# Kernel tuning notes

Measured on AMD Instinct MI355X. Metric: run time of the kernel, lower is better.

The kernel has to match this reference:

```python
import jax, jax.numpy as jnp
import numpy as np
import math

B, C, H, T, S = 2, 1024, 16, 2048, 2048
DH = C // H  # 64


def setup_inputs() -> dict:
    key = jax.random.key(0)
    ks = jax.random.split(key, 10)
    target = jax.random.normal(ks[0], (B, C, T), dtype=jnp.float32)
    source = jax.random.normal(ks[1], (B, C, S), dtype=jnp.float32)
    target_mask = (jax.random.uniform(ks[2], (B, 1, T)) < 0.9).astype(jnp.float32)
    source_mask = (jax.random.uniform(ks[3], (B, 1, S)) < 0.9).astype(jnp.float32)
    scale = 1.0 / math.sqrt(C)
    Wq = jax.random.normal(ks[4], (C, C), dtype=jnp.float32) * scale
    bq = jnp.zeros((C,), dtype=jnp.float32)
    Wk = jax.random.normal(ks[5], (C, C), dtype=jnp.float32) * scale
    bk = jnp.zeros((C,), dtype=jnp.float32)
    Wv = jax.random.normal(ks[6], (C, C), dtype=jnp.float32) * scale
    bv = jnp.zeros((C,), dtype=jnp.float32)
    return {"target": target, "source": source, "target_mask": target_mask,
            "source_mask": source_mask, "Wq": Wq, "bq": bq, "Wk": Wk, "bk": bk,
            "Wv": Wv, "bv": bv}


def _proj(W, b, x):
    # 1x1 Conv1d == pointwise channel mixing: [B,C,L] -> [B,C,L]
    return jnp.einsum('oc,bcl->bol', W, x) + b[None, :, None]


def reference(target, source, target_mask, source_mask, Wq, bq, Wk, bk, Wv, bv):
    q = _proj(Wq, bq, target).reshape(B, H, DH, T)
    k = _proj(Wk, bk, source).reshape(B, H, DH, S)
    v = _proj(Wv, bv, source).reshape(B, H, DH, S)
    # dot: [B,H,T,S], scaled by sqrt(d_head) (key.size(2) in torch)
    dot = jnp.einsum('bhdt,bhds->bhts', q, k) / math.sqrt(DH)
    # available mask [B,1,T,S], broadcast over heads
    avail = jnp.einsum('bjt,bjs->bjts', target_mask, source_mask)
    dot = avail * dot - (1.0 - avail) * 1.0e6
    # NOTE: original torch code overwrites the masked amap with a plain
    # softmax of the (masked) dot; we reproduce that exactly.
    amap = jax.nn.softmax(dot, axis=-1)
    out = jnp.einsum('bhts,bhds->bhdt', amap, v)  # [B,H,DH,T]
    return out.reshape(B, C, T)
```

## Files before the change

### kernel.cpp

```cpp
#include <hip/hip_runtime.h>

#define BB 2
#define CC 1024
#define HH 16
#define TT 2048
#define SS 2048
#define LL 2048
#define C2MASK 1442695.0f
#define NT_TILES (SS / 64)

typedef unsigned short u16;
typedef unsigned int u32;
typedef __attribute__((ext_vector_type(8))) short short8;
typedef __attribute__((ext_vector_type(4))) float f32x4;
typedef __attribute__((ext_vector_type(4))) unsigned short us4;
typedef __attribute__((ext_vector_type(2))) unsigned int u32x2;
typedef __attribute__((ext_vector_type(4))) unsigned int u32x4;

__device__ __forceinline__ u16 f2bf(float f) {
    union { float f; unsigned int i; } x; x.f = f;
    unsigned int r = x.i + 0x7FFFu + ((x.i >> 16) & 1u);
    return (u16)(r >> 16);
}
__device__ __forceinline__ float exp2_hw(float x) {
    float r;
    asm("v_exp_f32 %0, %1" : "=v"(r) : "v"(x));
    return r;
}
__device__ __forceinline__ float max3f(float a, float b, float c) {
    float r;
    asm("v_max3_f32 %0, %1, %2, %3" : "=v"(r) : "v"(a), "v"(b), "v"(c));
    return r;
}
__device__ __forceinline__ u32 cvtpk_bf16(float lo, float hi) {
    u32 r;
    asm("v_cvt_pk_bf16_f32 %0, %1, %2" : "=v"(r) : "v"(lo), "v"(hi));
    return r;
}
__device__ __forceinline__ void gload_lds16(const u16* g, u16* l) {
    __builtin_amdgcn_global_load_lds(
        (const __attribute__((address_space(1))) unsigned int*)g,
        (__attribute__((address_space(3))) unsigned int*)l, 16, 0, 0);
}

__global__ __launch_bounds__(256) void prep(
    const float* __restrict__ target, const float* __restrict__ source,
    const float* __restrict__ smaskp,
    const float* __restrict__ Wq, const float* __restrict__ Wk, const float* __restrict__ Wv,
    u16* __restrict__ Wb, u16* __restrict__ Tt, u16* __restrict__ St,
    float* __restrict__ sbias, float* __restrict__ zrow)
{
    __shared__ float xs[64][65];
    const int tid = threadIdx.x;
    const int bid = blockIdx.x;

    if (bid < 2048) {
        const int img  = bid >> 9;
        const int tile = bid & 511;
        const int ct = tile >> 5, lt = tile & 31;
        const int c0 = ct * 64, l0 = lt * 64;
        const float* src = ((img < 2) ? target : source) + (size_t)(img & 1) * CC * LL;
        u16* dst = ((img < 2) ? Tt : St) + (size_t)(img & 1) * LL * CC;

        const int i = tid >> 2, seg = (tid & 3) * 16;
        const float* g = src + (size_t)(c0 + i) * LL + l0 + seg;
        f32x4 a0 = *(const f32x4*)g;
        f32x4 a1 = *(const f32x4*)(g + 4);
        f32x4 a2 = *(const f32x4*)(g + 8);
        f32x4 a3 = *(const f32x4*)(g + 12);
#pragma unroll
        for (int j = 0; j < 4; j++) {
            xs[i][seg + j]      = a0[j];
            xs[i][seg + 4 + j]  = a1[j];
            xs[i][seg + 8 + j]  = a2[j];
            xs[i][seg + 12 + j] = a3[j];
        }
        __syncthreads();

        const int l = tid >> 2, cseg = (tid & 3) * 16;
        float f[16];
#pragma unroll
        for (int j = 0; j < 16; j++) f[j] = xs[cseg + j][l];
        u32x4 o0, o1;
#pragma unroll
        for (int k = 0; k < 4; k++) {
            o0[k] = cvtpk_bf16(f[2 * k], f[2 * k + 1]);
            o1[k] = cvtpk_bf16(f[8 + 2 * k], f[9 + 2 * k]);
        }
        u16* d = dst + (size_t)(l0 + l) * CC + c0 + cseg;
        *(u32x4*)d = o0;
        *(u32x4*)(d + 8) = o1;
    } else {
        const int wblk = bid - 2048;
        const size_t idx = (size_t)wblk * 2048 + tid * 8;
        const int m = (int)(idx >> 20);
        const size_t rem = idx & 1048575;
        const float* srcp = ((m == 0) ? Wq : (m == 1) ? Wk : Wv) + rem;
        f32x4 a = *(const f32x4*)srcp;
        f32x4 c = *(const f32x4*)(srcp + 4);
        u32x4 o;
        o[0] = cvtpk_bf16(a[0], a[1]); o[1] = cvtpk_bf16(a[2], a[3]);
        o[2] = cvtpk_bf16(c[0], c[1]); o[3] = cvtpk_bf16(c[2], c[3]);
        *(u32x4*)(Wb + ((size_t)m << 20) + rem) = o;

        if (wblk < 2) {
            const int b = wblk;
            const float* sm = smaskp + (size_t)b * SS;
            float* sb = sbias + (size_t)b * SS;
            for (int s = tid; s < SS; s += 256) {
                sb[s] = (sm[s] > 0.5f) ? 0.0f : -C2MASK;
                if (b == 0) zrow[s] = 0.0f;
            }
        }
    }
}

__global__ __launch_bounds__(512, 2) void qkv_gemm(
    const u16* __restrict__ Wb, const u16* __restrict__ Tt, const u16* __restrict__ St,
    const float* __restrict__ bq, const float* __restrict__ bk, const float* __restrict__ bv,
    const float* __restrict__ tmaskp,
    u16* __restrict__ Qb, u16* __restrict__ Kb, u16* __restrict__ Vb)
{
    __shared__ __align__(16) u16 As[2][16384];
    __shared__ __align__(16) u16 Bs[2][16384];

    const int orig = blockIdx.x;
    const int wg   = (orig & 7) * 24 + (orig >> 3);
    const int mT   = wg >> 4;
    const int nT   = wg & 15;
    const int m0 = mT * 256;
    const int n0 = nT * 256;
    const int p  = m0 >> 10;

    const u16* A  = Wb + (size_t)m0 * CC;
    const u16* Bx = ((p == 0) ? Tt : St) + (size_t)n0 * CC;
    const float* bias = (p == 0) ? bq : (p == 1) ? bk : bv;

    const int tid  = threadIdx.x;
    const int lane = tid & 63;
    const int wid  = tid >> 6;
    const int ln   = lane & 15;
    const int q    = lane >> 4;
    const int wm   = (wid >> 2) * 128;
    const int wn   = (wid & 3) * 64;

    const u16* ag[4]; const u16* bg[4];
#pragma unroll
    for (int e = 0; e < 4; e++) {
        const int s = tid + e * 512;
        const int row = s >> 3;
        const int c = (s & 7) ^ (row & 7);
        ag[e] = A  + (size_t)row * CC + c * 8;
        bg[e] = Bx + (size_t)row * CC + c * 8;
    }
    const int lw = wid * 512;

#define QSTAGE(buf, k0) do {                                   \
        gload_lds16(ag[0] + (k0), &As[buf][lw]);               \
        gload_lds16(ag[1] + (k0), &As[buf][4096 + lw]);        \
        gload_lds16(ag[2] + (k0), &As[buf][8192 + lw]);        \
        gload_lds16(ag[3] + (k0), &As[buf][12288 + lw]);       \
        gload_lds16(bg[0] + (k0), &Bs[buf][lw]);               \
        gload_lds16(bg[1] + (k0), &Bs[buf][4096 + lw]);        \
        gload_lds16(bg[2] + (k0), &Bs[buf][8192 + lw]);        \
        gload_lds16(bg[3] + (k0), &Bs[buf][12288 + lw]);       \
    } while (0)

    f32x4 acc[8][4];
#pragma unroll
    for (int i = 0; i < 8; i++)
#pragma unroll
        for (int j = 0; j < 4; j++) acc[i][j] = (f32x4){0.f, 0.f, 0.f, 0.f};

    const int sx0 = ((q ^ (ln & 7)) << 3);
    const int sx1 = (((q + 4) ^ (ln & 7)) << 3);

    QSTAGE(0, 0);

    int cur = 0;
    for (int ks = 0; ks < 16; ++ks) {
        __syncthreads();
        if (ks + 1 < 16) QSTAGE(cur ^ 1, (ks + 1) * 64);

        const u16* AsB = As[cur];
        const u16* BsB = Bs[cur];

        short8 bF[4][2];
#pragma unroll
        for (int nt = 0; nt < 4; nt++) {
            const u16* br = BsB + (wn + nt * 16 + ln) * 64;
            bF[nt][0] = *(const short8*)(br + sx0);
            bF[nt][1] = *(const short8*)(br + sx1);
        }
#pragma unroll
        for (int mt = 0; mt < 8; mt++) {
            const u16* ar = AsB + (wm + mt * 16 + ln) * 64;
            short8 a0 = *(const short8*)(ar + sx0);
            short8 a1 = *(const short8*)(ar + sx1);
#pragma unroll
            for (int nt = 0; nt < 4; nt++) {
                acc[mt][nt] = __builtin_amdgcn_mfma_f32_16x16x32_bf16(a0, bF[nt][0], acc[mt][nt], 0, 0, 0);
                acc[mt][nt] = __builtin_amdgcn_mfma_f32_16x16x32_bf16(a1, bF[nt][1], acc[mt][nt], 0, 0, 0);
            }
        }
        cur ^= 1;
    }
#undef QSTAGE

    const float oscale = 0.18033688011112042f;
#pragma unroll
    for (int mt = 0; mt < 8; mt++) {
        const int o_base = (m0 & 1023) + wm + mt * 16 + q * 4;
        float bsf[4];
#pragma unroll
        for (int r = 0; r < 4; r++) bsf[r] = bias[o_base + r];
#pragma unroll
        for (int nt = 0; nt < 4; nt++) {
            const int l  = n0 + wn + nt * 16 + ln;
            const int b  = l >> 11;
            const int tk = l & 2047;
            if (p == 2) {
#pragma unroll
                for (int r = 0; r < 4; r++)
                    Vb[((size_t)b * CC + o_base + r) * SS + tk] = f2bf(acc[mt][nt][r] + bsf[r]);
            } else {
                const int h = o_base >> 6;
                const int d = o_base & 63;
                u16* dst = (p == 0) ? Qb : Kb;
                float sc2 = 1.0f;
                if (p == 0) sc2 = oscale * tmaskp[(size_t)b * TT + tk];
                us4 pk;
#pragma unroll
                for (int r = 0; r < 4; r++) pk[r] = (u16)f2bf((acc[mt][nt][r] + bsf[r]) * sc2);
                *(us4*)(dst + ((size_t)(b * HH + h) * TT + tk) * 64 + d) = pk;
            }
        }
    }
}

__global__ __launch_bounds__(512, 4) void attn_k(
    const u16* __restrict__ Qb, const u16* __restrict__ Kb, const u16* __restrict__ Vb,
    const float* __restrict__ tmask, const float* __restrict__ sbias,
    const float* __restrict__ zrow, float* __restrict__ out)
{
    __shared__ __align__(16) u16 Ks[2][64 * 64];
    __shared__ __align__(16) u16 Vs[2][64 * 64];
    __shared__ __align__(16) u16 Ps[8][16 * 64];

    const int tid  = threadIdx.x;
    const int wid  = tid >> 6;
    const int lane = tid & 63;
    const int ln   = lane & 15;
    const int q    = lane >> 4;

    const int idx   = blockIdx.x;
    const int xcd   = idx & 7;
    const int rest  = idx >> 3;
    const int ttile = rest & 15;
    const int bh    = (rest >> 4) * 8 + xcd;
    const int b     = bh >> 4;
    const int h     = bh & 15;
    const int t0    = ttile * 128 + wid * 16;

    const u16* Qp = Qb + (size_t)bh * TT * 64;
    const u16* Kp = Kb + (size_t)bh * SS * 64;
    const u16* Vp = Vb + ((size_t)b * CC + h * 64) * SS;

    const float tm = tmask[(size_t)b * TT + t0 + ln];
    const float* bp = (tm > 0.5f) ? (sbias + (size_t)b * SS) : zrow;

    const int r0  = tid >> 3;
    const int c0  = tid & 7;
    const int cs0 = c0 ^ (r0 & 7);
    const u16* kg = Kp + (size_t)r0 * 64 + cs0 * 8;
    const u16* vg = Vp + (size_t)r0 * SS + cs0 * 8;
    const int lws = wid * 512;

#define STAGE(buf, sn) do {                                 \
        gload_lds16(kg + (size_t)(sn) * 64, &Ks[buf][lws]); \
        gload_lds16(vg + (sn), &Vs[buf][lws]);              \
    } while (0)

    short8 qB0 = *(const short8*)(Qp + (size_t)(t0 + ln) * 64 + q * 8);
    short8 qB1 = *(const short8*)(Qp + (size_t)(t0 + ln) * 64 + 32 + q * 8);

    float mR = -3.0e38f, lR = 0.f;
    f32x4 oA[4];
#pragma unroll
    for (int dt = 0; dt < 4; dt++) oA[dt] = (f32x4){0.f, 0.f, 0.f, 0.f};

    const int sx0 = ((q ^ (ln & 7)) << 3);
    const int sx1 = (((q + 4) ^ (ln & 7)) << 3);

    u16* pw = Ps[wid];

    STAGE(0, 0);

    int cur = 0;
#pragma unroll 2
    for (int it = 0; it < NT_TILES; ++it) {
        const int s0 = it * 64;
        __syncthreads();
        if (it + 1 < NT_TILES) STAGE(cur ^ 1, s0 + 64);

        const u16* KsB = Ks[cur];
        const u16* VsB = Vs[cur];

        f32x4 sc[4];
        __builtin_amdgcn_s_setprio(1);
#pragma unroll
        for (int nt = 0; nt < 4; nt++) {
            const u16* kr = KsB + (nt * 16 + ln) * 64;
            short8 k0 = *(const short8*)(kr + sx0);
            short8 k1 = *(const short8*)(kr + sx1);
            f32x4 bias = *(const f32x4*)(bp + s0 + nt * 16 + q * 4);
            sc[nt] = __builtin_amdgcn_mfma_f32_16x16x32_bf16(k0, qB0, bias, 0, 0, 0);
            sc[nt] = __builtin_amdgcn_mfma_f32_16x16x32_bf16(k1, qB1, sc[nt], 0, 0, 0);
        }
        __builtin_amdgcn_s_setprio(0);

        float m4[4];
#pragma unroll
        for (int nt = 0; nt < 4; nt++)
            m4[nt] = fmaxf(max3f(sc[nt][0], sc[nt][1], sc[nt][2]), sc[nt][3]);
        float m_ = fmaxf(max3f(m4[0], m4[1], m4[2]), m4[3]);
        m_ = fmaxf(m_, __shfl_xor(m_, 16, 64));
        m_ = fmaxf(m_, __shfl_xor(m_, 32, 64));

        if (!__all(m_ - mR <= 8.0f)) {
            const float mN = fmaxf(mR, m_);
            const float al = exp2_hw(mR - mN);
            lR *= al;
#pragma unroll
            for (int dt = 0; dt < 4; dt++) oA[dt] *= al;
            mR = mN;
        }

        float s4[4];
#pragma unroll
        for (int nt = 0; nt < 4; nt++) {
#pragma unroll
            for (int r = 0; r < 4; r++) sc[nt][r] = exp2_hw(sc[nt][r] - mR);
            s4[nt] = (sc[nt][0] + sc[nt][1]) + (sc[nt][2] + sc[nt][3]);
        }
        float s_ = (s4[0] + s4[1]) + (s4[2] + s4[3]);
        s_ += __shfl_xor(s_, 16, 64);
        s_ += __shfl_xor(s_, 32, 64);
        lR += s_;

#pragma unroll
        for (int nt = 0; nt < 4; nt++) {
            u32x2 w;
            w[0] = cvtpk_bf16(sc[nt][0], sc[nt][1]);
            w[1] = cvtpk_bf16(sc[nt][2], sc[nt][3]);
            const int chunk = (nt << 1) | (q >> 1);
            *(u32x2*)(pw + ln * 64 + ((chunk ^ (ln & 7)) << 3) + ((q & 1) << 2)) = w;
        }
        short8 pB0 = *(const short8*)(pw + ln * 64 + sx0);
        short8 pB1 = *(const short8*)(pw + ln * 64 + sx1);
        __builtin_amdgcn_s_setprio(1);
#pragma unroll
        for (int dt = 0; dt < 4; dt++) {
            const u16* vr = VsB + (dt * 16 + ln) * 64;
            short8 v0 = *(const short8*)(vr + sx0);
            short8 v1 = *(const short8*)(vr + sx1);
            oA[dt] = __builtin_amdgcn_mfma_f32_16x16x32_bf16(v0, pB0, oA[dt], 0, 0, 0);
            oA[dt] = __builtin_amdgcn_mfma_f32_16x16x32_bf16(v1, pB1, oA[dt], 0, 0, 0);
        }
        __builtin_amdgcn_s_setprio(0);
        cur ^= 1;
    }
#undef STAGE

    const float inv = 1.0f / lR;
#pragma unroll
    for (int dt = 0; dt < 4; dt++)
#pragma unroll
        for (int r = 0; r < 4; r++)
            out[((size_t)b * CC + h * 64 + dt * 16 + q * 4 + r) * TT + t0 + ln] =
                oA[dt][r] * inv;
}

extern "C" void kernel_launch(void* const* d_in, const int* in_sizes, int n_in,
                              void* d_out, int out_size, void* d_ws, size_t ws_size,
                              hipStream_t stream)
{
    const float* target = (const float*)d_in[0];
    const float* source = (const float*)d_in[1];
    const float* tmask  = (const float*)d_in[2];
    const float* smask  = (const float*)d_in[3];
    const float* Wq = (const float*)d_in[4];
    const float* bq = (const float*)d_in[5];
    const float* Wk = (const float*)d_in[6];
    const float* bk = (const float*)d_in[7];
    const float* Wv = (const float*)d_in[8];
    const float* bv = (const float*)d_in[9];

    u16* ws = (u16*)d_ws;
    const size_t N1 = (size_t)BB * CC * TT;
    u16* Qb = ws;
    u16* Kb = ws + N1;
    u16* Vb = ws + 2 * N1;
    float* sbias = (float*)(ws + 3 * N1);
    float* zrow  = sbias + 2 * SS;
    u16* Wb = (u16*)(zrow + SS);
    u16* Tt = Wb + 3u * 1048576u;
    u16* St = Tt + (size_t)BB * LL * CC;

    prep<<<dim3(3584, 1, 1), dim3(256, 1, 1), 0, stream>>>(
        target, source, smask, Wq, Wk, Wv, Wb, Tt, St, sbias, zrow);
    qkv_gemm<<<dim3(192, 1, 1), dim3(512, 1, 1), 0, stream>>>(
        Wb, Tt, St, bq, bk, bv, tmask, Qb, Kb, Vb);
    attn_k<<<dim3(BB*HH*(TT/128), 1, 1), dim3(512, 1, 1), 0, stream>>>(
        Qb, Kb, Vb, tmask, sbias, zrow, (float*)d_out);
}
```

Measured before the change: 202.8 us.

## Interleave projection GEMM loads with MFMA phases and defer softmax row-sum reduction

Restructures the projection GEMM main loop into four phases. Each phase reads A/B fragments from LDS, issues part of the next tile's global-to-LDS staging, and runs a quarter of the MFMAs between explicit s_barriers and waitcnts, with raised wave priority around the MFMAs. The goal is to overlap global loads and LDS reads with matrix math instead of staging everything up front. Separately, the attention kernel keeps a per-lane partial row sum and does the cross-lane shuffle reduction once after the loop instead of every tile. Risks include extra barriers per K step, higher register pressure, and reliance on manual waitcnt ordering for correctness.

```diff
diff --git a/kernel.cpp b/kernel.cpp
--- a/kernel.cpp
+++ b/kernel.cpp
@@ -155,16 +155,8 @@
     }
     const int lw = wid * 512;
 
-#define QSTAGE(buf, k0) do {                                   \
-        gload_lds16(ag[0] + (k0), &As[buf][lw]);               \
-        gload_lds16(ag[1] + (k0), &As[buf][4096 + lw]);        \
-        gload_lds16(ag[2] + (k0), &As[buf][8192 + lw]);        \
-        gload_lds16(ag[3] + (k0), &As[buf][12288 + lw]);       \
-        gload_lds16(bg[0] + (k0), &Bs[buf][lw]);               \
-        gload_lds16(bg[1] + (k0), &Bs[buf][4096 + lw]);        \
-        gload_lds16(bg[2] + (k0), &Bs[buf][8192 + lw]);        \
-        gload_lds16(bg[3] + (k0), &Bs[buf][12288 + lw]);       \
-    } while (0)
+#define STG_A(buf, k0, e)  gload_lds16(ag[e] + (k0), &As[buf][(e) * 4096 + lw])
+#define STG_B(buf, k0, e)  gload_lds16(bg[e] + (k0), &Bs[buf][(e) * 4096 + lw])
 
     f32x4 acc[8][4];
 #pragma unroll
@@ -175,37 +167,70 @@
     const int sx0 = ((q ^ (ln & 7)) << 3);
     const int sx1 = (((q + 4) ^ (ln & 7)) << 3);
 
-    QSTAGE(0, 0);
-
-    int cur = 0;
-    for (int ks = 0; ks < 16; ++ks) {
-        __syncthreads();
-        if (ks + 1 < 16) QSTAGE(cur ^ 1, (ks + 1) * 64);
-
-        const u16* AsB = As[cur];
-        const u16* BsB = Bs[cur];
-
-        short8 bF[4][2];
-#pragma unroll
-        for (int nt = 0; nt < 4; nt++) {
-            const u16* br = BsB + (wn + nt * 16 + ln) * 64;
-            bF[nt][0] = *(const short8*)(br + sx0);
-            bF[nt][1] = *(const short8*)(br + sx1);
-        }
-#pragma unroll
-        for (int mt = 0; mt < 8; mt++) {
-            const u16* ar = AsB + (wm + mt * 16 + ln) * 64;
-            short8 a0 = *(const short8*)(ar + sx0);
-            short8 a1 = *(const short8*)(ar + sx1);
-#pragma unroll
-            for (int nt = 0; nt < 4; nt++) {
-                acc[mt][nt] = __builtin_amdgcn_mfma_f32_16x16x32_bf16(a0, bF[nt][0], acc[mt][nt], 0, 0, 0);
-                acc[mt][nt] = __builtin_amdgcn_mfma_f32_16x16x32_bf16(a1, bF[nt][1], acc[mt][nt], 0, 0, 0);
-            }
-        }
-        cur ^= 1;
+    short8 aQ[4][2];
+    short8 bQ[2][2][2];
+
+#define PH_READ_A(cb, base_mt) do {                                        \
+    _Pragma("unroll") for (int mt = 0; mt < 4; mt++) {                     \
+        const u16* ar = &As[cb][(wm + ((base_mt) + mt) * 16 + ln) * 64];   \
+        aQ[mt][0] = *(const short8*)(ar + sx0);                            \
+        aQ[mt][1] = *(const short8*)(ar + sx1); } } while (0)
+#define PH_READ_B(cb, ntg) do {                                            \
+    _Pragma("unroll") for (int nt = 0; nt < 2; nt++) {                     \
+        const u16* br = &Bs[cb][(wn + ((ntg) * 2 + nt) * 16 + ln) * 64];   \
+        bQ[ntg][nt][0] = *(const short8*)(br + sx0);                       \
+        bQ[ntg][nt][1] = *(const short8*)(br + sx1); } } while (0)
+#define PH_MFMA(mbase, ntg) do {                                           \
+    __builtin_amdgcn_s_setprio(1);                                         \
+    _Pragma("unroll") for (int mt = 0; mt < 4; mt++)                       \
+    _Pragma("unroll") for (int nt = 0; nt < 2; nt++) {                     \
+        acc[(mbase) + mt][(ntg) * 2 + nt] = __builtin_amdgcn_mfma_f32_16x16x32_bf16( \
+            aQ[mt][0], bQ[ntg][nt][0], acc[(mbase) + mt][(ntg) * 2 + nt], 0, 0, 0);  \
+        acc[(mbase) + mt][(ntg) * 2 + nt] = __builtin_amdgcn_mfma_f32_16x16x32_bf16( \
+            aQ[mt][1], bQ[ntg][nt][1], acc[(mbase) + mt][(ntg) * 2 + nt], 0, 0, 0); } \
+    __builtin_amdgcn_s_setprio(0); } while (0)
+#define LGKM0 do { asm volatile("s_waitcnt lgkmcnt(0)" ::: "memory");      \
+                   __builtin_amdgcn_sched_barrier(0); } while (0)
+#define VMDRAIN do { asm volatile("s_waitcnt vmcnt(0)" ::: "memory");      \
+                     __builtin_amdgcn_sched_barrier(0); } while (0)
+
+    STG_A(0, 0, 0); STG_A(0, 0, 1); STG_A(0, 0, 2); STG_A(0, 0, 3);
+    STG_B(0, 0, 0); STG_B(0, 0, 1); STG_B(0, 0, 2); STG_B(0, 0, 3);
+    __syncthreads();
+
+#pragma unroll 1
+    for (int T = 0; T < 16; ++T) {
+        const int c  = T & 1;
+        const int kn = (T + 1) * 64;
+        const bool stg = (T < 15);
+
+        PH_READ_A(c, 0); PH_READ_B(c, 0);
+        if (stg) { STG_A(c ^ 1, kn, 0); STG_A(c ^ 1, kn, 1);
+                   STG_A(c ^ 1, kn, 2); STG_A(c ^ 1, kn, 3); }
+        __builtin_amdgcn_s_barrier(); LGKM0; PH_MFMA(0, 0);
+        __builtin_amdgcn_s_barrier();
+
+        PH_READ_B(c, 1);
+        if (stg) { STG_B(c ^ 1, kn, 0); STG_B(c ^ 1, kn, 1);
+                   STG_B(c ^ 1, kn, 2); STG_B(c ^ 1, kn, 3); }
+        __builtin_amdgcn_s_barrier(); LGKM0; PH_MFMA(0, 1);
+        __builtin_amdgcn_s_barrier();
+
+        PH_READ_A(c, 4);
+        __builtin_amdgcn_s_barrier(); LGKM0; PH_MFMA(4, 0);
+        __builtin_amdgcn_s_barrier();
+
+        PH_MFMA(4, 1);
+        VMDRAIN;
+        __builtin_amdgcn_s_barrier();
     }
-#undef QSTAGE
+#undef VMDRAIN
+#undef LGKM0
+#undef PH_MFMA
+#undef PH_READ_B
+#undef PH_READ_A
+#undef STG_B
+#undef STG_A
 
     const float oscale = 0.18033688011112042f;
 #pragma unroll
@@ -343,10 +368,7 @@
             for (int r = 0; r < 4; r++) sc[nt][r] = exp2_hw(sc[nt][r] - mR);
             s4[nt] = (sc[nt][0] + sc[nt][1]) + (sc[nt][2] + sc[nt][3]);
         }
-        float s_ = (s4[0] + s4[1]) + (s4[2] + s4[3]);
-        s_ += __shfl_xor(s_, 16, 64);
-        s_ += __shfl_xor(s_, 32, 64);
-        lR += s_;
+        lR += (s4[0] + s4[1]) + (s4[2] + s4[3]);
 
 #pragma unroll
         for (int nt = 0; nt < 4; nt++) {
@@ -372,6 +394,8 @@
     }
 #undef STAGE
 
+    lR += __shfl_xor(lR, 16, 64);
+    lR += __shfl_xor(lR, 32, 64);
     const float inv = 1.0f / lR;
 #pragma unroll
     for (int dt = 0; dt < 4; dt++)
```

Result: no change. 201.8 us (-0.5%).
